# Optimization experiments

Hardware: AMD Instinct MI355X
Metric: run time of the kernel (lower is better)

The kernel has to match this reference:

```python
import jax, jax.numpy as jnp
import numpy as np

N = 50000   # nodes of ntype 'A'
E = 800000  # edges per metapath
M = 4       # metapaths (first-order, tail = 'A')
H = 4       # attn heads
C = 32      # out_channels = output_dim // attn_heads
IN = 256    # input_dim
D = H * C   # output_dim = 128
NEG_SLOPE = 0.2


def setup_inputs() -> dict:
    key = jax.random.key(0)
    ks = jax.random.split(key, 8)
    feats = jax.random.normal(ks[0], (N, IN), dtype=jnp.float32)
    edge_index = jax.random.randint(ks[1], (M, 2, E), 0, N, dtype=jnp.int32)
    W = jax.random.normal(ks[2], (IN, D), dtype=jnp.float32) * (2.0 / (IN + D)) ** 0.5
    b = jnp.zeros((D,), dtype=jnp.float32)
    attn = jax.random.normal(ks[3], (M, H, 2 * C), dtype=jnp.float32) * 0.1
    rel_attn_l = jax.random.normal(ks[4], (H, C), dtype=jnp.float32) * 0.1
    rel_attn_r = jax.random.normal(ks[5], (M + 1, H, C), dtype=jnp.float32) * 0.1
    rel_attn_bias = jnp.zeros((M + 1,), dtype=jnp.float32)
    return {"feats": feats, "edge_index": edge_index, "W": W, "b": b,
            "attn": attn, "rel_attn_l": rel_attn_l, "rel_attn_r": rel_attn_r,
            "rel_attn_bias": rel_attn_bias}


def _segment_softmax(logits, seg, num_segments):
    # logits: [E, H], seg: [E] target-node ids; softmax over incoming edges per node.
    seg_max = jax.ops.segment_max(logits, seg, num_segments=num_segments)  # [N, H]
    e = jnp.exp(logits - seg_max[seg])
    seg_sum = jax.ops.segment_sum(e, seg, num_segments=num_segments)       # [N, H]
    return e / (seg_sum[seg] + 1e-16)


def reference(feats, edge_index, W, b, attn, rel_attn_l, rel_attn_r, rel_attn_bias):
    # projection: per-ntype Linear + relu, reshape to heads
    h = jax.nn.relu(feats @ W + b).reshape(N, H, C)  # l_dict == r_dict == h

    # per-metapath GAT-style propagate (aggr='add')
    rels = []
    for m in range(M):
        src = edge_index[m, 0]
        dst = edge_index[m, 1]
        x_j = h[src]  # [E, H, C] source messages
        x_i = h[dst]  # [E, H, C] target queries
        # alpha = (cat([x_i, x_j], -1) * attn[m]).sum(-1), LeakyReLU(0.2)
        logits = jnp.einsum('ehc,hc->eh', x_i, attn[m, :, :C]) \
               + jnp.einsum('ehc,hc->eh', x_j, attn[m, :, C:])
        logits = jax.nn.leaky_relu(logits, NEG_SLOPE)
        alpha = _segment_softmax(logits, dst, N)                 # [E, H]
        out = jax.ops.segment_sum(x_j * alpha[..., None], dst, num_segments=N)  # [N, H, C]
        rels.append(out)
    rels.append(h)  # last relation slot = self (embedding[:, -1] = l_dict[ntype])
    emb = jnp.stack(rels, axis=1)  # [N, M+1, H, C]

    # beta relation-attention weights
    beta_l = jax.nn.relu(h * rel_attn_l)                          # [N, H, C]
    beta_r = jax.nn.relu(emb * rel_attn_r)                        # [N, M+1, H, C]
    beta = jnp.einsum('nhc,nrhc->nrh', beta_l, beta_r) + rel_attn_bias[None, :, None]
    beta = jax.nn.softmax(beta, axis=1)                           # over relations

    emb = (emb * beta[..., None]).sum(axis=1).reshape(N, D)
    return jax.nn.relu(emb)
```

## Files before the change

### kernel.cpp

```cpp
#include <hip/hip_runtime.h>
#include <math.h>

#define kN 50000
#define kE 800000
#define kM 4
#define kH 4
#define kC 32
#define kIN 256
#define kD 128

typedef __attribute__((ext_vector_type(8))) short bf16x8;
typedef __attribute__((ext_vector_type(4))) float f32x4;

__device__ __forceinline__ unsigned int f2bf_pack(float a, float b) {
    unsigned ua = __float_as_uint(a);
    ua += 0x7fffu + ((ua >> 16) & 1u);
    unsigned ub = __float_as_uint(b);
    ub += 0x7fffu + ((ub >> 16) & 1u);
    return (ua >> 16) | (ub & 0xffff0000u);
}
__device__ __forceinline__ unsigned short f2bf(float x) {
    unsigned u = __float_as_uint(x);
    u += 0x7fffu + ((u >> 16) & 1u);
    return (unsigned short)(u >> 16);
}

#define NBK 98
#define BCAP 10240
#define MW (NBK * BCAP)
#define PAB ((kE + 4095) / 4096)

__global__ void k_wcast(const float* __restrict__ W, unsigned short* __restrict__ Wt16) {
    const int col = blockIdx.x;
    const int k = threadIdx.x;
    Wt16[(size_t)col * kIN + k] = f2bf(W[(size_t)k * kD + col]);
}

#define GEMMB ((kN + 127) / 128)
__global__ __launch_bounds__(256) void k_gemmbucket(const float* __restrict__ feats,
                                                    const unsigned short* __restrict__ Wt16,
                                                    const float* __restrict__ b,
                                                    const float* __restrict__ attn,
                                                    unsigned short* __restrict__ h16,
                                                    float* __restrict__ sl,
                                                    float* __restrict__ sr,
                                                    const int* __restrict__ ei,
                                                    int* __restrict__ bcur,
                                                    unsigned int* __restrict__ pairs) {
    __shared__ unsigned short fr16[128 * 32];
    __shared__ unsigned short hlds[128][130];
    __shared__ int hist[NBK], h2[NBK], base_s[NBK];
    const int t = threadIdx.x;

    if (blockIdx.x >= GEMMB) {
        const int bi = blockIdx.x - GEMMB;
        const int m = bi / PAB;
        const int chunk = bi - m * PAB;
        const int e0 = chunk * 4096;
        for (int j = t; j < NBK; j += 256) { hist[j] = 0; h2[j] = 0; }
        __syncthreads();
        int src[16], dst[16];
#pragma unroll
        for (int i = 0; i < 16; i++) {
            const int e = e0 + i * 256 + t;
            const int eok = (e < kE) ? e : 0;
            src[i] = ei[(size_t)m * 2 * kE + eok];
            dst[i] = (e < kE) ? ei[(size_t)m * 2 * kE + kE + eok] : -1;
        }
#pragma unroll
        for (int i = 0; i < 16; i++)
            if (dst[i] >= 0) atomicAdd(&hist[dst[i] >> 9], 1);
        __syncthreads();
        for (int j = t; j < NBK; j += 256)
            base_s[j] = atomicAdd(&bcur[m * NBK + j], hist[j]);
        __syncthreads();
#pragma unroll
        for (int i = 0; i < 16; i++) {
            if (dst[i] >= 0) {
                const int bk = dst[i] >> 9;
                const int slot = base_s[bk] + atomicAdd(&h2[bk], 1);
                pairs[(size_t)m * MW + (size_t)bk * BCAP + slot] =
                    ((unsigned int)(dst[i] & 511) << 16) | (unsigned int)src[i];
            }
        }
        return;
    }

    const int lane = t & 63;
    const int wave = t >> 6;
    const int q = lane >> 4;
    const int m16 = lane & 15;
    const int wrow = (wave >> 1) * 64;
    const int wcol = (wave & 1) * 64;
    const int rowbase = blockIdx.x * 128;

    f32x4 acc[4][4];
#pragma unroll
    for (int i = 0; i < 4; i++)
#pragma unroll
        for (int j = 0; j < 4; j++) acc[i][j] = (f32x4){0.f, 0.f, 0.f, 0.f};

    const int srow = t >> 3;
    const int sk4 = t & 7;

    for (int kc = 0; kc < kIN; kc += 32) {
        __syncthreads();
#pragma unroll
        for (int it = 0; it < 4; it++) {
            const int row = srow + it * 32;
            const int rg = rowbase + row;
            float4 v = make_float4(0.f, 0.f, 0.f, 0.f);
            if (rg < kN)
                v = *reinterpret_cast<const float4*>(feats + (size_t)rg * kIN + kc + sk4 * 4);
            uint2 p;
            p.x = f2bf_pack(v.x, v.y);
            p.y = f2bf_pack(v.z, v.w);
            *reinterpret_cast<uint2*>(&fr16[row * 32 + sk4 * 4]) = p;
        }
        __syncthreads();

        bf16x8 afr[4], bfr[4];
#pragma unroll
        for (int ri = 0; ri < 4; ri++)
            afr[ri] = *reinterpret_cast<const bf16x8*>(
                &fr16[(wrow + ri * 16 + m16) * 32 + q * 8]);
#pragma unroll
        for (int ci = 0; ci < 4; ci++)
            bfr[ci] = *reinterpret_cast<const bf16x8*>(
                Wt16 + (size_t)(wcol + ci * 16 + m16) * kIN + kc + q * 8);
#pragma unroll
        for (int ri = 0; ri < 4; ri++)
#pragma unroll
            for (int ci = 0; ci < 4; ci++)
                acc[ri][ci] = __builtin_amdgcn_mfma_f32_16x16x32_bf16(
                    afr[ri], bfr[ci], acc[ri][ci], 0, 0, 0);
    }

    float bcol[4];
#pragma unroll
    for (int ci = 0; ci < 4; ci++) bcol[ci] = b[wcol + ci * 16 + m16];

#pragma unroll
    for (int ri = 0; ri < 4; ri++) {
#pragma unroll
        for (int reg = 0; reg < 4; reg++) {
            const int row = wrow + ri * 16 + q * 4 + reg;
            const int rg = rowbase + row;
#pragma unroll
            for (int ci = 0; ci < 4; ci++) {
                const int col = wcol + ci * 16 + m16;
                const float v = fmaxf(acc[ri][ci][reg] + bcol[ci], 0.f);
                const unsigned short us = f2bf(v);
                hlds[row][col] = us;
                if (rg < kN)
                    h16[(size_t)rg * kD + col] = us;
            }
        }
    }
    __syncthreads();

    const unsigned int* hl32 = reinterpret_cast<const unsigned int*>(&hlds[0][0]);
#pragma unroll
    for (int it = 0; it < 2; it++) {
        const int task = it * 256 + t;
        const int hh = task >> 7;
        const int nl = task & 127;
        const int n = rowbase + nl;
        if (n < kN) {
            unsigned int u[16];
#pragma unroll
            for (int k = 0; k < 16; k++) u[k] = hl32[nl * 65 + hh * 16 + k];
            float f0[16], f1[16];
#pragma unroll
            for (int k = 0; k < 16; k++) {
                f0[k] = __uint_as_float(u[k] << 16);
                f1[k] = __uint_as_float(u[k] & 0xffff0000u);
            }
#pragma unroll
            for (int m = 0; m < kM; m++) {
                const float2* al = reinterpret_cast<const float2*>(attn + (m * kH + hh) * 2 * kC);
                const float2* ar = al + 16;
                float s0 = 0.f, s1 = 0.f;
#pragma unroll
                for (int k = 0; k < 16; k++) {
                    const float2 a = al[k], r = ar[k];
                    s0 += f0[k] * a.x + f1[k] * a.y;
                    s1 += f0[k] * r.x + f1[k] * r.y;
                }
                sl[(size_t)(m * kH + hh) * kN + n] = s0;
                sr[(size_t)(m * kH + hh) * kN + n] = s1;
            }
        }
    }
}

#define SORTB (kM * NBK)
__global__ __launch_bounds__(256) void k_sort(const unsigned int* __restrict__ pairs,
                                              const int* __restrict__ bcur,
                                              int* __restrict__ offs,
                                              int* __restrict__ cnta,
                                              int* __restrict__ srcsort) {
    __shared__ int hist[512], pref[512], h2[512], wt[4];
    const int t = threadIdx.x;
    const int m = blockIdx.x / NBK;
    const int bk = blockIdx.x - m * NBK;
    const int bs = bk << 9;
    const int base = bk * BCAP;
    const int n = bcur[m * NBK + bk];
    const unsigned int* __restrict__ pb = pairs + (size_t)m * MW + base;
    int* __restrict__ ss = srcsort + (size_t)m * MW + base;

    hist[t] = 0; hist[t + 256] = 0; h2[t] = 0; h2[t + 256] = 0;
    __syncthreads();

    unsigned int v[40];
#pragma unroll
    for (int j = 0; j < 40; j++) {
        const int idx = j * 256 + t;
        v[j] = (idx < n) ? pb[idx] : 0xffffffffu;
    }
#pragma unroll
    for (int j = 0; j < 40; j++)
        if (v[j] != 0xffffffffu) atomicAdd(&hist[v[j] >> 16], 1);
    __syncthreads();

    const int lane = t & 63, wid = t >> 6;
    const int j0 = 2 * t, j1 = 2 * t + 1;
    const int h0 = hist[j0], h1 = hist[j1];
    const int s = h0 + h1;
    int incl = s;
#pragma unroll
    for (int d = 1; d < 64; d <<= 1) {
        const int x = __shfl_up(incl, d);
        if (lane >= d) incl += x;
    }
    if (lane == 63) wt[wid] = incl;
    __syncthreads();
    int woff = 0;
#pragma unroll
    for (int i = 0; i < 4; i++)
        if (i < wid) woff += wt[i];
    const int excl = woff + incl - s;
    pref[j0] = excl;
    pref[j1] = excl + h0;
    const int d0 = bs + j0, d1 = bs + j1;
    if (d0 < kN) { offs[m * kN + d0] = base + excl;       cnta[m * kN + d0] = h0; }
    if (d1 < kN) { offs[m * kN + d1] = base + excl + h0;  cnta[m * kN + d1] = h1; }
    __syncthreads();

#pragma unroll
    for (int j = 0; j < 40; j++) {
        if (v[j] != 0xffffffffu) {
            const int dl = (int)(v[j] >> 16);
            const int pos = pref[dl] + atomicAdd(&h2[dl], 1);
            ss[pos] = (int)(v[j] & 0xffffu);
        }
    }
}

#define CH 16

#define AGG_BODY(GN)                                                            \
    {                                                                           \
        int sj[GN];                                                             \
        _Pragma("unroll")                                                       \
        for (int j = 0; j < GN; j++) {                                          \
            const int id = __builtin_amdgcn_readlane(my0, j);                   \
            sj[j] = (j < nb) ? id : dst;                                        \
        }                                                                       \
        unsigned int u[GN];                                                     \
        _Pragma("unroll")                                                       \
        for (int j = 0; j < GN; j++)                                            \
            u[j] = *reinterpret_cast<const unsigned int*>(                      \
                hb + (((size_t)(unsigned int)sj[j] << 8) + ebyte));             \
        float x = sl_h + srv;                                                   \
        x = x > 0.f ? x : 0.2f * x;                         \
        const float w = (c + jj < cnt) ? __expf(x) : 0.f;                       \
        sum += w;                                                               \
        swtsH[m][l] = w;                                                        \
        __builtin_amdgcn_wave_barrier();                                        \
        const float4 w0 = *reinterpret_cast<const float4*>(&swtsH[m][hh * 16]); \
        const float4 w1 = *reinterpret_cast<const float4*>(&swtsH[m][hh*16+4]); \
        const float4 w2 = *reinterpret_cast<const float4*>(&swtsH[m][hh*16+8]); \
        const float4 w3 = *reinterpret_cast<const float4*>(&swtsH[m][hh*16+12]);\
        __builtin_amdgcn_wave_barrier();                                        \
        my0 = my1;                                                              \
        my1 = sbase[c + 2 * CH + jj];                                           \
        srv = srb[my0];                                                         \
        const float wj[16] = {w0.x, w0.y, w0.z, w0.w, w1.x, w1.y, w1.z, w1.w,   \
                              w2.x, w2.y, w2.z, w2.w, w3.x, w3.y, w3.z, w3.w};  \
        _Pragma("unroll")                                                       \
        for (int j = 0; j < GN; j++) {                                          \
            a0 += wj[j] * __uint_as_float(u[j] << 16);                          \
            a1 += wj[j] * __uint_as_float(u[j] & 0xffff0000u);                  \
        }                                                                       \
    }

__global__ __launch_bounds__(512) void k_agg(const unsigned short* __restrict__ h16,
                                             const float* __restrict__ sl,
                                             const float* __restrict__ sr,
                                             const int* __restrict__ offs,
                                             const int* __restrict__ cnta,
                                             const int* __restrict__ srcsort,
                                             const float* __restrict__ ral,
                                             const float* __restrict__ rar,
                                             const float* __restrict__ rbias,
                                             float* __restrict__ out) {
    const int t = threadIdx.x;
    const int hv = t >> 8;
    const int dst = blockIdx.x * 2 + hv;
    const int m = (t >> 6) & 3;
    const int l = t & 63;
    const int hh = l >> 4;
    const int jj = l & 15;
    const int e0 = l * 2;

    __shared__ float smres[2][kM][kD];
    __shared__ float swts[2][kM][64];
    float (* __restrict__ smresH)[kD] = smres[hv];
    float (* __restrict__ swtsH)[64] = swts[hv];

    const int beg = offs[m * kN + dst];
    const int cnt = cnta[m * kN + dst];
    const float sl_h = sl[(size_t)(m * kH + hh) * kN + dst];
    const int* __restrict__ sbase = srcsort + (size_t)m * MW + beg;
    const char* __restrict__ hb = (const char*)h16;
    const float* __restrict__ srb = sr + (size_t)(m * kH + hh) * kN;
    const unsigned int ebyte = (unsigned int)(e0 << 1);

    float sum = 0.f, a0 = 0.f, a1 = 0.f;

    int my0 = sbase[jj];
    int my1 = sbase[CH + jj];
    float srv = srb[my0];

    for (int c = 0; c < cnt; c += CH) {
        const int nb = cnt - c;
        if (nb >= 9) AGG_BODY(16) else AGG_BODY(8)
    }

    sum += __shfl_xor(sum, 1);
    sum += __shfl_xor(sum, 2);
    sum += __shfl_xor(sum, 4);
    sum += __shfl_xor(sum, 8);
    const float inv = 1.0f / (sum + 1e-16f);
    smresH[m][e0] = a0 * inv;
    smresH[m][e0 + 1] = a1 * inv;
    __syncthreads();

    if (m == 0) {
        const unsigned int ud = *reinterpret_cast<const unsigned int*>(
            hb + (((unsigned int)dst << 8) + ebyte));
        const float hd0 = __uint_as_float(ud << 16);
        const float hd1 = __uint_as_float(ud & 0xffff0000u);
        const float bl0 = fmaxf(hd0 * ral[e0], 0.f);
        const float bl1 = fmaxf(hd1 * ral[e0 + 1], 0.f);
        float emb0[5], emb1[5], beta[5];
#pragma unroll
        for (int r = 0; r < 5; r++) {
            const float x0 = (r < 4) ? smresH[r][e0] : hd0;
            const float x1 = (r < 4) ? smresH[r][e0 + 1] : hd1;
            emb0[r] = x0;
            emb1[r] = x1;
            const float br0 = fmaxf(x0 * rar[r * kD + e0], 0.f);
            const float br1 = fmaxf(x1 * rar[r * kD + e0 + 1], 0.f);
            float p = bl0 * br0 + bl1 * br1;
            p += __shfl_xor(p, 1);
            p += __shfl_xor(p, 2);
            p += __shfl_xor(p, 4);
            p += __shfl_xor(p, 8);
            beta[r] = p + rbias[r];
        }
        float mx = beta[0];
#pragma unroll
        for (int r = 1; r < 5; r++) mx = fmaxf(mx, beta[r]);
        float s = 0.f, wgt[5];
#pragma unroll
        for (int r = 0; r < 5; r++) { wgt[r] = __expf(beta[r] - mx); s += wgt[r]; }
        const float invb = 1.f / s;
        float o0 = 0.f, o1 = 0.f;
#pragma unroll
        for (int r = 0; r < 5; r++) { o0 += emb0[r] * wgt[r]; o1 += emb1[r] * wgt[r]; }
        out[(size_t)dst * kD + e0] = fmaxf(o0 * invb, 0.f);
        out[(size_t)dst * kD + e0 + 1] = fmaxf(o1 * invb, 0.f);
    }
}

extern "C" void kernel_launch(void* const* d_in, const int* in_sizes, int n_in,
                              void* d_out, int out_size, void* d_ws, size_t ws_size,
                              hipStream_t stream) {
    const float* feats = (const float*)d_in[0];
    const int* ei      = (const int*)d_in[1];
    const float* W     = (const float*)d_in[2];
    const float* b     = (const float*)d_in[3];
    const float* attn  = (const float*)d_in[4];
    const float* ral   = (const float*)d_in[5];
    const float* rar   = (const float*)d_in[6];
    const float* rbias = (const float*)d_in[7];
    float* out = (float*)d_out;

    char* ws = (char*)d_ws;
    size_t off = 0;
    auto alloc = [&](size_t bytes) -> void* {
        void* p = ws + off;
        off = (off + bytes + 255) & ~(size_t)255;
        return p;
    };
    unsigned short* h16 = (unsigned short*)alloc(sizeof(short) * (size_t)kN * kD);
    unsigned short* Wt16= (unsigned short*)alloc(sizeof(short) * (size_t)kD * kIN);
    float* sl   = (float*)alloc(sizeof(float) * (size_t)kM * kN * kH);
    float* sr   = (float*)alloc(sizeof(float) * (size_t)kM * kN * kH);
    int* cnta   = (int*)alloc(sizeof(int) * (size_t)kM * kN);
    int* offs   = (int*)alloc(sizeof(int) * (size_t)kM * kN);
    int* bcur   = (int*)alloc(sizeof(int) * (kM * NBK + 64));
    int* srcsort= (int*)alloc(sizeof(int) * ((size_t)kM * MW + 64));
    unsigned int* pairs = (unsigned int*)alloc(sizeof(int) * (size_t)kM * MW);

    hipMemsetAsync(bcur, 0, sizeof(int) * (kM * NBK + 64), stream);
    hipMemsetAsync(srcsort, 0, sizeof(int) * ((size_t)kM * MW + 64), stream);
    k_wcast<<<kD, kIN, 0, stream>>>(W, Wt16);
    k_gemmbucket<<<GEMMB + kM * PAB, 256, 0, stream>>>(feats, Wt16, b, attn,
                                                       h16, sl, sr, ei, bcur, pairs);
    k_sort<<<SORTB, 256, 0, stream>>>(pairs, bcur, offs, cnta, srcsort);
    k_agg<<<kN / 2, 512, 0, stream>>>(h16, sl, sr, offs, cnta, srcsort,
                                      ral, rar, rbias, out);
}
```

Measured before the change: 383.9 us.

## Interleave heads in attention-score arrays and use one node per aggregation block

The per-node attention scores sl/sr are stored node-major with heads interleaved ([M][N][H]) instead of head-major, so a gathered source node's score for all heads sits in one 16-byte chunk. The aggregation kernel now handles one destination node per 256-thread block instead of two per 512-thread block. The layout change aims to improve cache-line reuse on the random sr gathers. Smaller blocks may also reduce barrier coupling between two destinations with different degrees. In exchange, the score-writing stage in the GEMM kernel now uses a different task mapping and the aggregation launches twice as many blocks.

```diff
diff --git a/kernel.cpp b/kernel.cpp
--- a/kernel.cpp
+++ b/kernel.cpp
@@ -163,8 +163,8 @@
 #pragma unroll
     for (int it = 0; it < 2; it++) {
         const int task = it * 256 + t;
-        const int hh = task >> 7;
-        const int nl = task & 127;
+        const int hh = task & 3;
+        const int nl = task >> 2;
         const int n = rowbase + nl;
         if (n < kN) {
             unsigned int u[16];
@@ -187,8 +187,8 @@
                     s0 += f0[k] * a.x + f1[k] * a.y;
                     s1 += f0[k] * r.x + f1[k] * r.y;
                 }
-                sl[(size_t)(m * kH + hh) * kN + n] = s0;
-                sr[(size_t)(m * kH + hh) * kN + n] = s1;
+                sl[((size_t)m * kN + n) * kH + hh] = s0;
+                sr[((size_t)m * kN + n) * kH + hh] = s1;
             }
         }
     }
@@ -277,16 +277,17 @@
         x = x > 0.f ? x : 0.2f * x;                         \
         const float w = (c + jj < cnt) ? __expf(x) : 0.f;                       \
         sum += w;                                                               \
-        swtsH[m][l] = w;                                                        \
+        swts[m][l] = w;                                                         \
         __builtin_amdgcn_wave_barrier();                                        \
-        const float4 w0 = *reinterpret_cast<const float4*>(&swtsH[m][hh * 16]); \
-        const float4 w1 = *reinterpret_cast<const float4*>(&swtsH[m][hh*16+4]); \
-        const float4 w2 = *reinterpret_cast<const float4*>(&swtsH[m][hh*16+8]); \
-        const float4 w3 = *reinterpret_cast<const float4*>(&swtsH[m][hh*16+12]);\
+        const float4 w0 = *reinterpret_cast<const float4*>(&swts[m][hh * 16]);  \
+        const float4 w1 = *reinterpret_cast<const float4*>(&swts[m][hh*16+4]);  \
+        const float4 w2 = *reinterpret_cast<const float4*>(&swts[m][hh*16+8]);  \
+        const float4 w3 = *reinterpret_cast<const float4*>(&swts[m][hh*16+12]); \
         __builtin_amdgcn_wave_barrier();                                        \
         my0 = my1;                                                              \
         my1 = sbase[c + 2 * CH + jj];                                           \
-        srv = srb[my0];                                                         \
+        srv = *reinterpret_cast<const float*>(                                  \
+            srb + (((unsigned int)my0 << 4) + hbyte));                          \
         const float wj[16] = {w0.x, w0.y, w0.z, w0.w, w1.x, w1.y, w1.z, w1.w,   \
                               w2.x, w2.y, w2.z, w2.w, w3.x, w3.y, w3.z, w3.w};  \
         _Pragma("unroll")                                                       \
@@ -296,7 +297,7 @@
         }                                                                       \
     }
 
-__global__ __launch_bounds__(512) void k_agg(const unsigned short* __restrict__ h16,
+__global__ __launch_bounds__(256) void k_agg(const unsigned short* __restrict__ h16,
                                              const float* __restrict__ sl,
                                              const float* __restrict__ sr,
                                              const int* __restrict__ offs,
@@ -306,33 +307,32 @@
                                              const float* __restrict__ rar,
                                              const float* __restrict__ rbias,
                                              float* __restrict__ out) {
+    const int dst = blockIdx.x;
     const int t = threadIdx.x;
-    const int hv = t >> 8;
-    const int dst = blockIdx.x * 2 + hv;
-    const int m = (t >> 6) & 3;
+    const int m = t >> 6;
     const int l = t & 63;
     const int hh = l >> 4;
     const int jj = l & 15;
     const int e0 = l * 2;
 
-    __shared__ float smres[2][kM][kD];
-    __shared__ float swts[2][kM][64];
-    float (* __restrict__ smresH)[kD] = smres[hv];
-    float (* __restrict__ swtsH)[64] = swts[hv];
+    __shared__ float smres[kM][kD];
+    __shared__ float swts[kM][64];
 
     const int beg = offs[m * kN + dst];
     const int cnt = cnta[m * kN + dst];
-    const float sl_h = sl[(size_t)(m * kH + hh) * kN + dst];
+    const float sl_h = sl[((size_t)m * kN + dst) * kH + hh];
     const int* __restrict__ sbase = srcsort + (size_t)m * MW + beg;
     const char* __restrict__ hb = (const char*)h16;
-    const float* __restrict__ srb = sr + (size_t)(m * kH + hh) * kN;
+    const char* __restrict__ srb = (const char*)(sr + (size_t)m * kN * kH);
     const unsigned int ebyte = (unsigned int)(e0 << 1);
+    const unsigned int hbyte = (unsigned int)(hh << 2);
 
     float sum = 0.f, a0 = 0.f, a1 = 0.f;
 
     int my0 = sbase[jj];
     int my1 = sbase[CH + jj];
-    float srv = srb[my0];
+    float srv = *reinterpret_cast<const float*>(
+        srb + (((unsigned int)my0 << 4) + hbyte));
 
     for (int c = 0; c < cnt; c += CH) {
         const int nb = cnt - c;
@@ -344,8 +344,8 @@
     sum += __shfl_xor(sum, 4);
     sum += __shfl_xor(sum, 8);
     const float inv = 1.0f / (sum + 1e-16f);
-    smresH[m][e0] = a0 * inv;
-    smresH[m][e0 + 1] = a1 * inv;
+    smres[m][e0] = a0 * inv;
+    smres[m][e0 + 1] = a1 * inv;
     __syncthreads();
 
     if (m == 0) {
@@ -358,8 +358,8 @@
         float emb0[5], emb1[5], beta[5];
 #pragma unroll
         for (int r = 0; r < 5; r++) {
-            const float x0 = (r < 4) ? smresH[r][e0] : hd0;
-            const float x1 = (r < 4) ? smresH[r][e0 + 1] : hd1;
+            const float x0 = (r < 4) ? smres[r][e0] : hd0;
+            const float x1 = (r < 4) ? smres[r][e0 + 1] : hd1;
             emb0[r] = x0;
             emb1[r] = x1;
             const float br0 = fmaxf(x0 * rar[r * kD + e0], 0.f);
@@ -422,6 +422,6 @@
     k_gemmbucket<<<GEMMB + kM * PAB, 256, 0, stream>>>(feats, Wt16, b, attn,
                                                        h16, sl, sr, ei, bcur, pairs);
     k_sort<<<SORTB, 256, 0, stream>>>(pairs, bcur, offs, cnta, srcsort);
-    k_agg<<<kN / 2, 512, 0, stream>>>(h16, sl, sr, offs, cnta, srcsort,
-                                      ral, rar, rbias, out);
-}
+    k_agg<<<kN, 256, 0, stream>>>(h16, sl, sr, offs, cnta, srcsort,
+                                  ral, rar, rbias, out);
+}
```

After: 349.5 us. 9.0% less time.
